# Optimization experiments

Hardware: AMD Instinct MI355X
Metric: run time of the kernel (lower is better)

The kernel has to match this reference:

```python
import jax, jax.numpy as jnp
import numpy as np

EMBED_DIM = 1024
NUM_HEADS = 16
HEAD_DIM = EMBED_DIM // NUM_HEADS


def setup_inputs() -> dict:
    key = jax.random.key(0)
    ks = jax.random.split(key, 9)
    B, S, E = 2, 2048, EMBED_DIM
    scale = 1.0 / np.sqrt(E)
    x = jax.random.normal(ks[0], (B, S, E), dtype=jnp.float32)
    Wq = jax.random.normal(ks[1], (E, E), dtype=jnp.float32) * scale
    bq = jax.random.normal(ks[2], (E,), dtype=jnp.float32) * 0.01
    Wk = jax.random.normal(ks[3], (E, E), dtype=jnp.float32) * scale
    bk = jax.random.normal(ks[4], (E,), dtype=jnp.float32) * 0.01
    Wv = jax.random.normal(ks[5], (E, E), dtype=jnp.float32) * scale
    bv = jax.random.normal(ks[6], (E,), dtype=jnp.float32) * 0.01
    Wo = jax.random.normal(ks[7], (E, E), dtype=jnp.float32) * scale
    bo = jax.random.normal(ks[8], (E,), dtype=jnp.float32) * 0.01
    return {"x": x, "Wq": Wq, "bq": bq, "Wk": Wk, "bk": bk,
            "Wv": Wv, "bv": bv, "Wo": Wo, "bo": bo}


def reference(x, Wq, bq, Wk, bk, Wv, bv, Wo, bo):
    B, S, E = x.shape
    H, D = NUM_HEADS, HEAD_DIM
    # projections (torch Linear: x @ W.T + b), reshape to (B, H, S, D)
    q = (x @ Wq.T + bq).reshape(B, S, H, D).transpose(0, 2, 1, 3)
    k = (x @ Wk.T + bk).reshape(B, S, H, D).transpose(0, 2, 1, 3)
    v = (x @ Wv.T + bv).reshape(B, S, H, D).transpose(0, 2, 1, 3)
    softmax_scale = 1.0 / np.sqrt(D)
    # (B, H, S, S) scores, causal mask, stable softmax
    scores = softmax_scale * jnp.einsum('bhsd,bhtd->bhst', q, k)
    causal = jnp.tril(jnp.ones((S, S), dtype=bool))  # True = keep
    scores = jnp.where(causal, scores, -jnp.inf)
    attn = jax.nn.softmax(scores, axis=-1)
    out = jnp.einsum('bhst,bhtd->bhsd', attn, v)  # (B, H, S, D)
    out = out.transpose(0, 2, 1, 3).reshape(B, S, E)
    return out @ Wo.T + bo
```

## Files before the change

### kernel.cpp

```cpp
#include <hip/hip_runtime.h>
#include <cstdint>
#include <cstddef>

#define SEQ   2048
#define BATCH 2
#define EMB   1024
#define NH    16
#define HD    64
#define MTOT  (BATCH * SEQ)
#define NX    (MTOT * EMB)
#define NW    (EMB * EMB)
#define QS    3072
#define SLOTF 8448
#define NSLOT 1152

typedef __bf16 bf16_t;
typedef __bf16 bf16x2 __attribute__((ext_vector_type(2)));
typedef __bf16 bf16x4 __attribute__((ext_vector_type(4)));
typedef __bf16 bf16x8 __attribute__((ext_vector_type(8)));
typedef float  f32x4  __attribute__((ext_vector_type(4)));
typedef float  f32x16 __attribute__((ext_vector_type(16)));

typedef __attribute__((address_space(1))) const void* as1cv;
typedef __attribute__((address_space(3))) void*       as3v;

__device__ __forceinline__ void async_cp16(const void* g, void* l) {
  __builtin_amdgcn_global_load_lds((as1cv)g, (as3v)l, 16, 0, 0);
}

__device__ __forceinline__ f32x16 mfma32(bf16x8 a, bf16x8 b, f32x16 c) {
  return __builtin_amdgcn_mfma_f32_32x32x16_bf16(a, b, c, 0, 0, 0);
}

__device__ __forceinline__ uint32_t pk2(float a, float b) {
  bf16x2 t; t[0] = (bf16_t)a; t[1] = (bf16_t)b;
  return __builtin_bit_cast(uint32_t, t);
}
__device__ __forceinline__ bf16x8 mk_frag(uint32_t x, uint32_t y,
                                          uint32_t z, uint32_t w) {
  uint4 u; u.x = x; u.y = y; u.z = z; u.w = w;
  return __builtin_bit_cast(bf16x8, u);
}

__device__ __forceinline__ void plane_swap(uint32_t& a, uint32_t& b) {
  asm("v_permlane32_swap_b32 %0, %1" : "+v"(a), "+v"(b));
}

__global__ __launch_bounds__(256) void cvt_all(
    const float* __restrict__ x,  const float* __restrict__ wq,
    const float* __restrict__ wk, const float* __restrict__ wv,
    const float* __restrict__ wo,
    bf16_t* __restrict__ xb,  bf16_t* __restrict__ wqb,
    bf16_t* __restrict__ wkb, bf16_t* __restrict__ wvb,
    bf16_t* __restrict__ wob) {
  long e = ((long)blockIdx.x * 256 + threadIdx.x) * 4;
  const float* s; bf16_t* d; long off;
  if (e < NX) { s = x; d = xb; off = e; }
  else {
    long e2 = e - NX;
    int w = (int)(e2 >> 20);
    off = e2 & (NW - 1);
    s = (w == 0) ? wq : (w == 1) ? wk : (w == 2) ? wv : wo;
    d = (w == 0) ? wqb : (w == 1) ? wkb : (w == 2) ? wvb : wob;
  }
  float4 v = *(const float4*)(s + off);
  bf16x4 o;
  o[0] = (bf16_t)v.x; o[1] = (bf16_t)v.y; o[2] = (bf16_t)v.z; o[3] = (bf16_t)v.w;
  *(bf16x4*)(d + off) = o;
}

__global__ __launch_bounds__(256) void vtrans(const bf16_t* __restrict__ QKV,
                                              bf16_t* __restrict__ VT) {
  const int hb = blockIdx.x;
  const int sb = blockIdx.y;
  const int h = hb & 15, b = hb >> 4;
  const int t = threadIdx.x;
  __shared__ __align__(16) bf16_t Ts[64 * 72];
  const bf16_t* Vp = QKV + ((size_t)(b * SEQ + sb * 64)) * QS + 2048 + h * HD;
  const int sr = t >> 4, d0 = (t & 15) * 4;
#pragma unroll
  for (int i = 0; i < 4; ++i) {
    bf16x4 v = *(const bf16x4*)(Vp + (size_t)(sr + 16 * i) * QS + d0);
    *(bf16x4*)&Ts[(sr + 16 * i) * 72 + d0] = v;
  }
  __syncthreads();
  const int d = t >> 2, tc = (t & 3) * 16;
  __align__(16) bf16_t out[16];
#pragma unroll
  for (int j = 0; j < 16; ++j) out[j] = Ts[(tc + j) * 72 + d];
  bf16_t* dst = VT + ((size_t)hb * HD + d) * SEQ + sb * 64 + tc;
  *(uint4*)(dst)     = *(uint4*)&out[0];
  *(uint4*)(dst + 8) = *(uint4*)&out[8];
}

template <typename OT, int BN, int CS>
__global__ __launch_bounds__(256) void gemm_f(
    const bf16_t* __restrict__ A, const bf16_t* __restrict__ Bw,
    const float* __restrict__ b0, const float* __restrict__ b1,
    const float* __restrict__ b2, OT* __restrict__ C) {
  constexpr int K = EMB, BK = 64;
  __shared__ __align__(16) bf16_t As[128 * BK];
  __shared__ __align__(16) bf16_t Bs[BN * BK];

  const int tid  = threadIdx.x;
  const int lane = tid & 63;
  const int wave = tid >> 6;
  const int l31  = lane & 31;
  const int hi   = lane >> 5;
  const int wm   = (wave >> 1) * 64;
  const int wn   = (wave & 1) * (BN / 2);
  const int m0   = blockIdx.y * 128;
  const int n0   = blockIdx.x * BN;

  const float* bias = (n0 < 1024) ? b0 : ((n0 < 2048) ? b1 : b2);

  const int row0 = tid >> 3, slot = tid & 7;
  const bf16_t* gA[4];
  const bf16_t* gB[BN / 32];
#pragma unroll
  for (int i = 0; i < 4; ++i)
    gA[i] = A + (size_t)(m0 + row0 + 32 * i) * K + (slot ^ (row0 & 7)) * 8;
#pragma unroll
  for (int i = 0; i < BN / 32; ++i)
    gB[i] = Bw + (size_t)(n0 + row0 + 32 * i) * K + (slot ^ (row0 & 7)) * 8;

  f32x16 acc[2][BN / 64] = {};
  const int sw = l31 & 7;

  for (int kk = 0; kk < K; kk += BK) {
#pragma unroll
    for (int i = 0; i < 4; ++i)
      async_cp16(gA[i] + kk, &As[(tid + 256 * i) * 8]);
#pragma unroll
    for (int i = 0; i < BN / 32; ++i)
      async_cp16(gB[i] + kk, &Bs[(tid + 256 * i) * 8]);
    __syncthreads();

#pragma unroll
    for (int ks = 0; ks < 4; ++ks) {
      const int js = ((ks * 2 + hi) ^ sw) * 8;
      bf16x8 af[2], bfr[BN / 64];
#pragma unroll
      for (int i = 0; i < 2; ++i)
        af[i] = *(const bf16x8*)&As[(wm + i * 32 + l31) * BK + js];
#pragma unroll
      for (int j = 0; j < BN / 64; ++j)
        bfr[j] = *(const bf16x8*)&Bs[(wn + j * 32 + l31) * BK + js];
#pragma unroll
      for (int i = 0; i < 2; ++i)
#pragma unroll
        for (int j = 0; j < BN / 64; ++j)
          acc[i][j] = mfma32(af[i], bfr[j], acc[i][j]);
    }
    __syncthreads();
  }

#pragma unroll
  for (int i = 0; i < 2; ++i)
#pragma unroll
    for (int j = 0; j < BN / 64; ++j) {
      const int col = n0 + wn + j * 32 + l31;
      const float bv = bias[col & 1023];
#pragma unroll
      for (int r = 0; r < 16; ++r) {
        const int row = m0 + wm + i * 32 + (r & 3) + 8 * (r >> 2) + 4 * hi;
        C[(size_t)row * CS + col] = (OT)(acc[i][j][r] + bv);
      }
    }
}

__global__ __launch_bounds__(256, 3) void attn128(
    const bf16_t* __restrict__ QKVg, const bf16_t* __restrict__ VTg,
    bf16_t* __restrict__ Og, float* __restrict__ Pb) {
  static const unsigned char St[40] = {
      3, 7, 7, 10, 11, 11, 11, 14, 14, 15, 15, 15, 15,
      6, 6, 9, 9, 10, 10, 12, 12, 13, 13, 13, 13, 14, 14,
      2, 5, 5, 8, 8, 8, 9, 12, 12,
      4, 4, 1, 0};
  static const unsigned char Ct[40] = {
      0, 0, 1, 0, 0, 1, 2, 0, 1, 0, 1, 2, 3,
      0, 1, 0, 1, 1, 2, 0, 1, 0, 1, 2, 3, 2, 3,
      0, 0, 1, 0, 1, 2, 2, 2, 3,
      0, 1, 0, 0};
  static const unsigned char cum[12] = {0, 2, 4, 6, 8, 11, 14, 17, 20, 24, 28, 32};

  const int hb  = blockIdx.x;
  const int y   = blockIdx.y;
  const int s   = St[y], c = Ct[y];
  const int nit = 2 * s + 2;
  const int nch = (s >> 2) + 1;
  const int bse = nit / nch;
  const int rem = nit - bse * nch;
  const int len = bse + (c < rem ? 1 : 0);
  const int it0 = c * bse + (c < rem ? c : rem);
  const int h = hb & 15, b = hb >> 4;
  const int tid = threadIdx.x;
  const int lane = tid & 63, wave = tid >> 6;
  const int l31 = lane & 31, hi = lane >> 5;

  __shared__ __align__(16) bf16_t Ks[2][64 * 72];
  __shared__ __align__(16) bf16_t VsT[2][64 * 72];
  __shared__ __align__(16) bf16_t Qs[128 * 64];

  const size_t base = ((size_t)b * SEQ) * QS + (size_t)h * HD;
  const bf16_t* Qb  = QKVg + base;
  const bf16_t* Kp  = QKVg + base + 1024;
  const bf16_t* VTp = VTg + (size_t)hb * HD * SEQ;

  const int kr0r = tid >> 3, kcol = (tid & 7) * 8;
  const int kr1r = kr0r + 32;
  const int lo0 = kr0r * 72 + kcol;
  const int lo1 = lo0 + 32 * 72;

  const int q0  = s * 128;
  const bf16_t* Qp = Qb + (size_t)q0 * QS;

  const bf16_t* Kn0 = Kp + (size_t)it0 * 64 * QS;
  const bf16_t* Vn0 = VTp + it0 * 64;
  uint4 kr0 = *(const uint4*)(Kn0 + (size_t)kr0r * QS + kcol);
  uint4 kr1 = *(const uint4*)(Kn0 + (size_t)kr1r * QS + kcol);
  uint4 vr0 = *(const uint4*)(Vn0 + (size_t)kr0r * SEQ + kcol);
  uint4 vr1 = *(const uint4*)(Vn0 + (size_t)kr1r * SEQ + kcol);

#pragma unroll
  for (int i = 0; i < 4; ++i) {
    const int cc = tid + 256 * i;
    *(uint4*)&Qs[(cc >> 3) * 64 + (cc & 7) * 8] =
        *(const uint4*)(Qp + (size_t)(cc >> 3) * QS + (cc & 7) * 8);
  }
  __syncthreads();

  bf16x8 qf[4];
#pragma unroll
  for (int kk = 0; kk < 4; ++kk)
    qf[kk] = *(const bf16x8*)&Qs[(32 * wave + l31) * 64 + kk * 16 + hi * 8];

  bf16x8 onef;
#pragma unroll
  for (int i = 0; i < 8; ++i) onef[i] = (bf16_t)1.0f;

  f32x16 acc_t0 = {}, acc_t1 = {};
  f32x16 acc_l  = {};

  for (int j = 0; j < len; ++j) {
    const int it = it0 + j;
    bf16_t* Kc = &Ks[j & 1][0];
    bf16_t* Vc = &VsT[j & 1][0];
    *(uint4*)&Kc[lo0] = kr0;
    *(uint4*)&Kc[lo1] = kr1;
    *(uint4*)&Vc[lo0] = vr0;
    *(uint4*)&Vc[lo1] = vr1;
    __syncthreads();

    if (j + 1 < len) {
      const bf16_t* Kn  = Kp + (size_t)(it + 1) * 64 * QS;
      const bf16_t* VTn = VTp + (it + 1) * 64;
      kr0 = *(const uint4*)(Kn + (size_t)kr0r * QS + kcol);
      kr1 = *(const uint4*)(Kn + (size_t)kr1r * QS + kcol);
      vr0 = *(const uint4*)(VTn + (size_t)kr0r * SEQ + kcol);
      vr1 = *(const uint4*)(VTn + (size_t)kr1r * SEQ + kcol);
    }

    const bool active = (64 * it <= q0 + 32 * wave + 31);
    if (active) {
      f32x16 s0 = {}, s1 = {};
      __builtin_amdgcn_s_setprio(1);
#pragma unroll
      for (int kk = 0; kk < 4; ++kk) {
        const bf16x8 kf0 = *(const bf16x8*)&Kc[l31 * 72 + kk * 16 + hi * 8];
        const bf16x8 kf1 =
            *(const bf16x8*)&Kc[(32 + l31) * 72 + kk * 16 + hi * 8];
        s0 = mfma32(kf0, qf[kk], s0);
        s1 = mfma32(kf1, qf[kk], s1);
      }
      __builtin_amdgcn_s_setprio(0);

      constexpr float SC2 = 0.18033688011112042f;
      if (it >= nit - 2) {
        const int qg = q0 + 32 * wave + l31;
        const int k0 = 64 * it + 4 * hi;
#pragma unroll
        for (int r = 0; r < 16; ++r) {
          const int key = k0 + (r & 3) + 8 * (r >> 2);
          float p0 = exp2f(__builtin_fmaf(s0[r], SC2, -8.f));
          float p1 = exp2f(__builtin_fmaf(s1[r], SC2, -8.f));
          if (key > qg) p0 = 0.f;
          if (key + 32 > qg) p1 = 0.f;
          s0[r] = p0; s1[r] = p1;
        }
      } else {
#pragma unroll
        for (int r = 0; r < 16; ++r) {
          s0[r] = exp2f(__builtin_fmaf(s0[r], SC2, -8.f));
          s1[r] = exp2f(__builtin_fmaf(s1[r], SC2, -8.f));
        }
      }

      bf16x8 pf[4];
#pragma unroll
      for (int kk = 0; kk < 4; ++kk) {
        const f32x16& g = (kk < 2) ? s0 : s1;
        const int bir = 8 * (kk & 1);
        uint32_t w0 = pk2(g[bir + 0], g[bir + 1]);
        uint32_t w1 = pk2(g[bir + 2], g[bir + 3]);
        uint32_t w2 = pk2(g[bir + 4], g[bir + 5]);
        uint32_t w3 = pk2(g[bir + 6], g[bir + 7]);
        plane_swap(w0, w2);
        plane_swap(w1, w3);
        pf[kk] = mk_frag(w0, w1, w2, w3);
      }

      __builtin_amdgcn_s_setprio(1);
#pragma unroll
      for (int kk = 0; kk < 4; ++kk) {
        const bf16x8 vf0 = *(const bf16x8*)&Vc[l31 * 72 + kk * 16 + hi * 8];
        const bf16x8 vf1 =
            *(const bf16x8*)&Vc[(32 + l31) * 72 + kk * 16 + hi * 8];
        acc_t0 = mfma32(vf0, pf[kk], acc_t0);
        acc_t1 = mfma32(vf1, pf[kk], acc_t1);
        acc_l  = mfma32(onef, pf[kk], acc_l);
      }
      __builtin_amdgcn_s_setprio(0);
    }
  }

  if (nch == 1) {
    const float inv = 1.f / acc_l[0];
    bf16_t* Ow = &Qs[(32 * wave) * 64];
#pragma unroll
    for (int aq = 0; aq < 4; ++aq)
#pragma unroll
      for (int cq = 0; cq < 4; cq += 2) {
        const int r = 4 * aq + cq;
        const int d = cq + 8 * aq + 4 * hi;
        *(uint32_t*)&Ow[l31 * 64 + d] =
            pk2(acc_t0[r] * inv, acc_t0[r + 1] * inv);
        *(uint32_t*)&Ow[l31 * 64 + d + 32] =
            pk2(acc_t1[r] * inv, acc_t1[r + 1] * inv);
      }
    bf16_t* Op = Og + ((size_t)b * SEQ + q0 + 32 * wave) * EMB + (size_t)h * HD;
#pragma unroll
    for (int i = 0; i < 4; ++i) {
      const int id = lane + 64 * i;
      const int row = id >> 3, col8 = (id & 7) * 8;
      *(uint4*)(Op + (size_t)row * EMB + col8) =
          *(const uint4*)&Ow[row * 64 + col8];
    }
  } else {
    float* P = Pb + (size_t)(hb * 36 + cum[s - 4] + c) * SLOTF;
#pragma unroll
    for (int i = 0; i < 4; ++i) {
      f32x4 v0, v1;
#pragma unroll
      for (int e = 0; e < 4; ++e) {
        v0[e] = acc_t0[4 * i + e];
        v1[e] = acc_t1[4 * i + e];
      }
      *(f32x4*)(P + (size_t)(i * 256 + tid) * 4)       = v0;
      *(f32x4*)(P + (size_t)((4 + i) * 256 + tid) * 4) = v1;
    }
    P[8192 + tid] = acc_l[0];
  }
}

__global__ __launch_bounds__(256) void attn_combine(
    const float* __restrict__ Pb, bf16_t* __restrict__ Og) {
  static const unsigned char cum[12] = {0, 2, 4, 6, 8, 11, 14, 17, 20, 24, 28, 32};
  const int hb = blockIdx.x, sp = blockIdx.y;
  const int s = sp + 4;
  const int h = hb & 15, b = hb >> 4;
  const int t = threadIdx.x;
  const int lane = t & 63, wave = t >> 6;
  const int l31 = lane & 31, hi = lane >> 5;
  const int nch = (s >> 2) + 1;
  const float* P0 = Pb + (size_t)(hb * 36 + cum[sp]) * SLOTF;

  f32x4 a[8] = {};
  float ls = 0.f;
  for (int c = 0; c < nch; ++c) {
    const float* P = P0 + (size_t)c * SLOTF;
#pragma unroll
    for (int i = 0; i < 8; ++i)
      a[i] += *(const f32x4*)(P + (size_t)(i * 256 + t) * 4);
    ls += P[8192 + t];
  }
  const float inv = 1.f / ls;

  __shared__ __align__(16) bf16_t Ow[128 * 64];
  bf16_t* Owp = &Ow[(32 * wave) * 64];
#pragma unroll
  for (int aq = 0; aq < 4; ++aq)
#pragma unroll
    for (int cq = 0; cq < 4; cq += 2) {
      const int d = cq + 8 * aq + 4 * hi;
      *(uint32_t*)&Owp[l31 * 64 + d] =
          pk2(a[aq][cq] * inv, a[aq][cq + 1] * inv);
      *(uint32_t*)&Owp[l31 * 64 + d + 32] =
          pk2(a[4 + aq][cq] * inv, a[4 + aq][cq + 1] * inv);
    }
  bf16_t* Op =
      Og + ((size_t)b * SEQ + 128 * s + 32 * wave) * EMB + (size_t)h * HD;
#pragma unroll
  for (int i = 0; i < 4; ++i) {
    const int id = lane + 64 * i;
    const int row = id >> 3, col8 = (id & 7) * 8;
    *(uint4*)(Op + (size_t)row * EMB + col8) =
        *(const uint4*)&Owp[row * 64 + col8];
  }
}

extern "C" void kernel_launch(void* const* d_in, const int* in_sizes, int n_in,
                              void* d_out, int out_size, void* d_ws,
                              size_t ws_size, hipStream_t stream) {
  const float* x  = (const float*)d_in[0];
  const float* Wq = (const float*)d_in[1];
  const float* bq = (const float*)d_in[2];
  const float* Wk = (const float*)d_in[3];
  const float* bk = (const float*)d_in[4];
  const float* Wv = (const float*)d_in[5];
  const float* bv = (const float*)d_in[6];
  const float* Wo = (const float*)d_in[7];
  const float* bo = (const float*)d_in[8];
  float* out = (float*)d_out;

  char* p = (char*)d_ws;
  bf16_t* xb   = (bf16_t*)p; p += (size_t)NX * 2;
  bf16_t* wqb  = (bf16_t*)p; p += (size_t)NW * 2;
  bf16_t* wkb  = (bf16_t*)p; p += (size_t)NW * 2;
  bf16_t* wvb  = (bf16_t*)p; p += (size_t)NW * 2;
  bf16_t* wob  = (bf16_t*)p; p += (size_t)NW * 2;
  bf16_t* qkvb = (bf16_t*)p; p += (size_t)NX * 3 * 2;
  bf16_t* ab   = (bf16_t*)p; p += (size_t)NX * 2;
  float*  pbuf = (float*)p;  p += (size_t)NSLOT * SLOTF * 4;
  bf16_t* vtb  = xb;

  const int ntot = NX + 4 * NW;
  cvt_all<<<dim3(ntot / 4 / 256), 256, 0, stream>>>(
      x, Wq, Wk, Wv, Wo, xb, wqb, wkb, wvb, wob);

  gemm_f<bf16_t, 128, QS><<<dim3(QS / 128, MTOT / 128), 256, 0, stream>>>(
      xb, wqb, bq, bk, bv, qkvb);

  vtrans<<<dim3(BATCH * NH, SEQ / 64), 256, 0, stream>>>(qkvb, vtb);

  attn128<<<dim3(BATCH * NH, 40), 256, 0, stream>>>(qkvb, vtb, ab, pbuf);

  attn_combine<<<dim3(BATCH * NH, 12), 256, 0, stream>>>(pbuf, ab);

  gemm_f<float, 64, EMB><<<dim3(EMB / 64, MTOT / 128), 256, 0, stream>>>(
      ab, wob, bo, bo, bo, out);
}
```

Before: 187.0 us.

## Replace QKV projection GEMM with 256x256-tile 8-wave pipelined kernel

Adds a new QKV projection GEMM that uses 256x256 output tiles, 512 threads (8 waves), and double-buffered LDS fed by async copies. Each K step is split into four phases that interleave prefetch of the next tile with MFMA work, using explicit barriers, vmcnt waits and s_setprio. The grid is also remapped so that blocks sharing data run close together. Larger tiles raise data reuse and the phased schedule is meant to hide global load latency, but the grid shrinks to 192 blocks and register and LDS pressure go up.

```diff
diff --git a/kernel.cpp b/kernel.cpp
--- a/kernel.cpp
+++ b/kernel.cpp
@@ -45,6 +45,9 @@
 __device__ __forceinline__ void plane_swap(uint32_t& a, uint32_t& b) {
   asm("v_permlane32_swap_b32 %0, %1" : "+v"(a), "+v"(b));
 }
+
+#define CFENCE asm volatile("" ::: "memory")
+#define BARRIER do { CFENCE; __builtin_amdgcn_s_barrier(); CFENCE; } while (0)
 
 __global__ __launch_bounds__(256) void cvt_all(
     const float* __restrict__ x,  const float* __restrict__ wq,
@@ -169,6 +172,120 @@
     }
 }
 
+__global__ __launch_bounds__(512, 2) void gemm8(
+    const bf16_t* __restrict__ A, const bf16_t* __restrict__ Bw,
+    const float* __restrict__ b0, const float* __restrict__ b1,
+    const float* __restrict__ b2, bf16_t* __restrict__ C) {
+  constexpr int K = EMB, BK = 64, NT = K / BK;
+  __shared__ __align__(16) bf16_t As[2][2][128 * BK];
+  __shared__ __align__(16) bf16_t Bs[2][2][128 * BK];
+
+  const int bid = blockIdx.y * 12 + blockIdx.x;
+  const int wg  = (bid & 7) * 24 + (bid >> 3);
+  const int bx  = wg >> 4, by = wg & 15;
+  const int n0  = bx * 256, m0 = by * 256;
+
+  const int tid  = threadIdx.x;
+  const int lane = tid & 63;
+  const int wave = tid >> 6;
+  const int l31  = lane & 31;
+  const int hi   = lane >> 5;
+  const int wm   = wave >> 2;
+  const int wn   = wave & 3;
+  const int sw   = l31 & 7;
+
+  const float* bias = (n0 < 1024) ? b0 : ((n0 < 2048) ? b1 : b2);
+
+  const int row = tid >> 3, slot = tid & 7;
+  const int scol = (slot ^ (row & 7)) * 8;
+  const bf16_t* gA[2][2];
+  const bf16_t* gB[2][2];
+#pragma unroll
+  for (int h = 0; h < 2; ++h)
+#pragma unroll
+    for (int i = 0; i < 2; ++i) {
+      gA[h][i] = A  + (size_t)(m0 + h * 128 + row + 64 * i) * K + scol;
+      gB[h][i] = Bw + (size_t)(n0 + h * 128 + row + 64 * i) * K + scol;
+    }
+
+#define STAGE_A8(par, h, kk) do {                                     \
+    async_cp16(gA[h][0] + (kk), &As[par][h][tid * 8]);                \
+    async_cp16(gA[h][1] + (kk), &As[par][h][(tid + 512) * 8]); } while (0)
+#define STAGE_B8(par, h, kk) do {                                     \
+    async_cp16(gB[h][0] + (kk), &Bs[par][h][tid * 8]);                \
+    async_cp16(gB[h][1] + (kk), &Bs[par][h][(tid + 512) * 8]); } while (0)
+
+  f32x16 acc[2][2][2] = {};
+
+#define PHASE8(qm, qn, STAGE_STMT, TAIL_STMT)                               \
+  do {                                                                      \
+    const bf16_t* Ab_ = &As[cur][wm][0];                                    \
+    const int bh_ = (wn * 64 + (qn) * 32) >> 7;                             \
+    const int br_ = ((wn * 64 + (qn) * 32) & 127) + l31;                    \
+    const bf16_t* Bb_ = &Bs[cur][bh_][0];                                   \
+    bf16x8 af0_[4], af1_[4], bf_[4];                                        \
+    _Pragma("unroll")                                                       \
+    for (int ks = 0; ks < 4; ++ks) {                                        \
+      const int js = ((ks * 2 + hi) ^ sw) * 8;                              \
+      af0_[ks] = *(const bf16x8*)&Ab_[((qm) * 64 + l31) * BK + js];         \
+      af1_[ks] = *(const bf16x8*)&Ab_[((qm) * 64 + 32 + l31) * BK + js];    \
+      bf_[ks]  = *(const bf16x8*)&Bb_[br_ * BK + js];                       \
+    }                                                                       \
+    STAGE_STMT;                                                             \
+    BARRIER;                                                                \
+    asm volatile("s_waitcnt lgkmcnt(0)" ::: "memory");                      \
+    __builtin_amdgcn_s_setprio(1);                                          \
+    _Pragma("unroll")                                                       \
+    for (int ks = 0; ks < 4; ++ks) {                                        \
+      acc[qm][0][qn] = mfma32(af0_[ks], bf_[ks], acc[qm][0][qn]);           \
+      acc[qm][1][qn] = mfma32(af1_[ks], bf_[ks], acc[qm][1][qn]);           \
+    }                                                                       \
+    __builtin_amdgcn_s_setprio(0);                                          \
+    TAIL_STMT;                                                              \
+    BARRIER;                                                                \
+  } while (0)
+
+  STAGE_B8(0, 0, 0);
+  STAGE_B8(0, 1, 0);
+  STAGE_A8(0, 0, 0);
+  STAGE_A8(0, 1, 0);
+  asm volatile("s_waitcnt vmcnt(2)" ::: "memory");
+  BARRIER;
+
+#pragma unroll 1
+  for (int t = 0; t < NT; ++t) {
+    const int cur = t & 1, nxt = cur ^ 1;
+    const int koff = (t + 1) * BK;
+    const bool pf = (t + 1 < NT);
+    PHASE8(0, 0, if (pf) STAGE_B8(nxt, 0, koff), );
+    PHASE8(0, 1, if (pf) STAGE_B8(nxt, 1, koff),
+           if (pf) { asm volatile("s_waitcnt vmcnt(4)" ::: "memory"); }
+           else    { asm volatile("s_waitcnt vmcnt(0)" ::: "memory"); });
+    PHASE8(1, 0, if (pf) STAGE_A8(nxt, 0, koff), );
+    PHASE8(1, 1, if (pf) STAGE_A8(nxt, 1, koff),
+           asm volatile("s_waitcnt vmcnt(2)" ::: "memory"));
+  }
+
+#pragma unroll
+  for (int qm = 0; qm < 2; ++qm)
+#pragma unroll
+    for (int f = 0; f < 2; ++f)
+#pragma unroll
+      for (int qn = 0; qn < 2; ++qn) {
+        const int col = n0 + wn * 64 + qn * 32 + l31;
+        const float bv = bias[col & 1023];
+#pragma unroll
+        for (int r = 0; r < 16; ++r) {
+          const int rw =
+              m0 + wm * 128 + qm * 64 + f * 32 + (r & 3) + 8 * (r >> 2) + 4 * hi;
+          C[(size_t)rw * QS + col] = (bf16_t)(acc[qm][f][qn][r] + bv);
+        }
+      }
+#undef PHASE8
+#undef STAGE_A8
+#undef STAGE_B8
+}
+
 __global__ __launch_bounds__(256, 3) void attn128(
     const bf16_t* __restrict__ QKVg, const bf16_t* __restrict__ VTg,
     bf16_t* __restrict__ Og, float* __restrict__ Pb) {
@@ -438,8 +555,7 @@
   cvt_all<<<dim3(ntot / 4 / 256), 256, 0, stream>>>(
       x, Wq, Wk, Wv, Wo, xb, wqb, wkb, wvb, wob);
 
-  gemm_f<bf16_t, 128, QS><<<dim3(QS / 128, MTOT / 128), 256, 0, stream>>>(
-      xb, wqb, bq, bk, bv, qkvb);
+  gemm8<<<dim3(12, 16), 512, 0, stream>>>(xb, wqb, bq, bk, bv, qkvb);
 
   vtrans<<<dim3(BATCH * NH, SEQ / 64), 256, 0, stream>>>(qkvb, vtb);
 
```

Result: slower. 199.4 us (+6.6%).

## Fuse split-K attention combine into last block and deepen K/V prefetch

Applied to the files above, without the earlier changes.

The attention main loop now keeps two register sets of K/V tiles, prefetching two iterations ahead. The next tile's LDS store is placed between the QK and PV phases, so each iteration needs one barrier instead of a store-then-sync pattern. The separate attn_combine kernel is removed: each split block writes its partials, bumps an atomic counter, and the last-arriving block sums the partials and writes the output. This saves a kernel launch and the re-read of its own partial, at the cost of extra registers, threadfence overhead and a counter reset in vtrans.

```diff
diff --git a/kernel.cpp b/kernel.cpp
--- a/kernel.cpp
+++ b/kernel.cpp
@@ -70,11 +70,16 @@
 }
 
 __global__ __launch_bounds__(256) void vtrans(const bf16_t* __restrict__ QKV,
-                                              bf16_t* __restrict__ VT) {
+                                              bf16_t* __restrict__ VT,
+                                              int* __restrict__ cnt) {
   const int hb = blockIdx.x;
   const int sb = blockIdx.y;
   const int h = hb & 15, b = hb >> 4;
   const int t = threadIdx.x;
+  if (hb == 0 && sb == 0) {
+    cnt[t] = 0;
+    if (t < 128) cnt[256 + t] = 0;
+  }
   __shared__ __align__(16) bf16_t Ts[64 * 72];
   const bf16_t* Vp = QKV + ((size_t)(b * SEQ + sb * 64)) * QS + 2048 + h * HD;
   const int sr = t >> 4, d0 = (t & 15) * 4;
@@ -171,7 +176,7 @@
 
 __global__ __launch_bounds__(256, 3) void attn128(
     const bf16_t* __restrict__ QKVg, const bf16_t* __restrict__ VTg,
-    bf16_t* __restrict__ Og, float* __restrict__ Pb) {
+    bf16_t* __restrict__ Og, float* __restrict__ Pb, int* __restrict__ cnt) {
   static const unsigned char St[40] = {
       3, 7, 7, 10, 11, 11, 11, 14, 14, 15, 15, 15, 15,
       6, 6, 9, 9, 10, 10, 12, 12, 13, 13, 13, 13, 14, 14,
@@ -201,6 +206,7 @@
   __shared__ __align__(16) bf16_t Ks[2][64 * 72];
   __shared__ __align__(16) bf16_t VsT[2][64 * 72];
   __shared__ __align__(16) bf16_t Qs[128 * 64];
+  __shared__ int oldS;
 
   const size_t base = ((size_t)b * SEQ) * QS + (size_t)h * HD;
   const bf16_t* Qb  = QKVg + base;
@@ -215,12 +221,18 @@
   const int q0  = s * 128;
   const bf16_t* Qp = Qb + (size_t)q0 * QS;
 
-  const bf16_t* Kn0 = Kp + (size_t)it0 * 64 * QS;
-  const bf16_t* Vn0 = VTp + it0 * 64;
-  uint4 kr0 = *(const uint4*)(Kn0 + (size_t)kr0r * QS + kcol);
-  uint4 kr1 = *(const uint4*)(Kn0 + (size_t)kr1r * QS + kcol);
-  uint4 vr0 = *(const uint4*)(Vn0 + (size_t)kr0r * SEQ + kcol);
-  uint4 vr1 = *(const uint4*)(Vn0 + (size_t)kr1r * SEQ + kcol);
+#define LOADT(itv, K0, K1, V0, V1) do {                                   \
+    const bf16_t* Kn_ = Kp + (size_t)(itv) * 64 * QS;                     \
+    const bf16_t* Vn_ = VTp + (size_t)(itv) * 64;                         \
+    K0 = *(const uint4*)(Kn_ + (size_t)kr0r * QS + kcol);                 \
+    K1 = *(const uint4*)(Kn_ + (size_t)kr1r * QS + kcol);                 \
+    V0 = *(const uint4*)(Vn_ + (size_t)kr0r * SEQ + kcol);                \
+    V1 = *(const uint4*)(Vn_ + (size_t)kr1r * SEQ + kcol);               \
+  } while (0)
+
+  uint4 kA0, kA1, vA0, vA1, kB0, kB1, vB0, vB1;
+  LOADT(it0, kA0, kA1, vA0, vA1);
+  LOADT(it0 + 1, kB0, kB1, vB0, vB1);
 
 #pragma unroll
   for (int i = 0; i < 4; ++i) {
@@ -228,6 +240,10 @@
     *(uint4*)&Qs[(cc >> 3) * 64 + (cc & 7) * 8] =
         *(const uint4*)(Qp + (size_t)(cc >> 3) * QS + (cc & 7) * 8);
   }
+  *(uint4*)&Ks[0][lo0] = kA0;
+  *(uint4*)&Ks[0][lo1] = kA1;
+  *(uint4*)&VsT[0][lo0] = vA0;
+  *(uint4*)&VsT[0][lo1] = vA1;
   __syncthreads();
 
   bf16x8 qf[4];
@@ -242,87 +258,88 @@
   f32x16 acc_t0 = {}, acc_t1 = {};
   f32x16 acc_l  = {};
 
-  for (int j = 0; j < len; ++j) {
-    const int it = it0 + j;
-    bf16_t* Kc = &Ks[j & 1][0];
-    bf16_t* Vc = &VsT[j & 1][0];
-    *(uint4*)&Kc[lo0] = kr0;
-    *(uint4*)&Kc[lo1] = kr1;
-    *(uint4*)&Vc[lo0] = vr0;
-    *(uint4*)&Vc[lo1] = vr1;
-    __syncthreads();
-
-    if (j + 1 < len) {
-      const bf16_t* Kn  = Kp + (size_t)(it + 1) * 64 * QS;
-      const bf16_t* VTn = VTp + (it + 1) * 64;
-      kr0 = *(const uint4*)(Kn + (size_t)kr0r * QS + kcol);
-      kr1 = *(const uint4*)(Kn + (size_t)kr1r * QS + kcol);
-      vr0 = *(const uint4*)(VTn + (size_t)kr0r * SEQ + kcol);
-      vr1 = *(const uint4*)(VTn + (size_t)kr1r * SEQ + kcol);
-    }
-
-    const bool active = (64 * it <= q0 + 32 * wave + 31);
-    if (active) {
-      f32x16 s0 = {}, s1 = {};
-      __builtin_amdgcn_s_setprio(1);
-#pragma unroll
-      for (int kk = 0; kk < 4; ++kk) {
-        const bf16x8 kf0 = *(const bf16x8*)&Kc[l31 * 72 + kk * 16 + hi * 8];
-        const bf16x8 kf1 =
-            *(const bf16x8*)&Kc[(32 + l31) * 72 + kk * 16 + hi * 8];
-        s0 = mfma32(kf0, qf[kk], s0);
-        s1 = mfma32(kf1, qf[kk], s1);
-      }
-      __builtin_amdgcn_s_setprio(0);
-
-      constexpr float SC2 = 0.18033688011112042f;
-      if (it >= nit - 2) {
-        const int qg = q0 + 32 * wave + l31;
-        const int k0 = 64 * it + 4 * hi;
-#pragma unroll
-        for (int r = 0; r < 16; ++r) {
-          const int key = k0 + (r & 3) + 8 * (r >> 2);
-          float p0 = exp2f(__builtin_fmaf(s0[r], SC2, -8.f));
-          float p1 = exp2f(__builtin_fmaf(s1[r], SC2, -8.f));
-          if (key > qg) p0 = 0.f;
-          if (key + 32 > qg) p1 = 0.f;
-          s0[r] = p0; s1[r] = p1;
-        }
-      } else {
-#pragma unroll
-        for (int r = 0; r < 16; ++r) {
-          s0[r] = exp2f(__builtin_fmaf(s0[r], SC2, -8.f));
-          s1[r] = exp2f(__builtin_fmaf(s1[r], SC2, -8.f));
-        }
-      }
-
-      bf16x8 pf[4];
-#pragma unroll
-      for (int kk = 0; kk < 4; ++kk) {
-        const f32x16& g = (kk < 2) ? s0 : s1;
-        const int bir = 8 * (kk & 1);
-        uint32_t w0 = pk2(g[bir + 0], g[bir + 1]);
-        uint32_t w1 = pk2(g[bir + 2], g[bir + 3]);
-        uint32_t w2 = pk2(g[bir + 4], g[bir + 5]);
-        uint32_t w3 = pk2(g[bir + 6], g[bir + 7]);
-        plane_swap(w0, w2);
-        plane_swap(w1, w3);
-        pf[kk] = mk_frag(w0, w1, w2, w3);
-      }
-
-      __builtin_amdgcn_s_setprio(1);
-#pragma unroll
-      for (int kk = 0; kk < 4; ++kk) {
-        const bf16x8 vf0 = *(const bf16x8*)&Vc[l31 * 72 + kk * 16 + hi * 8];
-        const bf16x8 vf1 =
-            *(const bf16x8*)&Vc[(32 + l31) * 72 + kk * 16 + hi * 8];
-        acc_t0 = mfma32(vf0, pf[kk], acc_t0);
-        acc_t1 = mfma32(vf1, pf[kk], acc_t1);
-        acc_l  = mfma32(onef, pf[kk], acc_l);
-      }
-      __builtin_amdgcn_s_setprio(0);
-    }
-  }
+#define ITER(jj, cb, CK0, CK1, CV0, CV1, NK0, NK1, NV0, NV1)              \
+  do {                                                                    \
+    const int it = it0 + (jj);                                            \
+    if ((jj) + 2 < len) LOADT(it + 2, CK0, CK1, CV0, CV1);                \
+    const bool active = (64 * it <= q0 + 32 * wave + 31);                 \
+    f32x16 s0 = {}, s1 = {};                                              \
+    bf16x8 pf[4];                                                         \
+    if (active) {                                                         \
+      __builtin_amdgcn_s_setprio(1);                                      \
+      _Pragma("unroll")                                                   \
+      for (int kk = 0; kk < 4; ++kk) {                                    \
+        const bf16x8 kf0 =                                                \
+            *(const bf16x8*)&Ks[cb][l31 * 72 + kk * 16 + hi * 8];         \
+        const bf16x8 kf1 =                                                \
+            *(const bf16x8*)&Ks[cb][(32 + l31) * 72 + kk * 16 + hi * 8];  \
+        s0 = mfma32(kf0, qf[kk], s0);                                     \
+        s1 = mfma32(kf1, qf[kk], s1);                                     \
+      }                                                                   \
+      __builtin_amdgcn_s_setprio(0);                                      \
+      constexpr float SC2 = 0.18033688011112042f;                         \
+      if (it >= nit - 2) {                                                \
+        const int qg = q0 + 32 * wave + l31;                              \
+        const int k0 = 64 * it + 4 * hi;                                  \
+        _Pragma("unroll")                                                 \
+        for (int r = 0; r < 16; ++r) {                                    \
+          const int key = k0 + (r & 3) + 8 * (r >> 2);                    \
+          float p0 = exp2f(__builtin_fmaf(s0[r], SC2, -8.f));             \
+          float p1 = exp2f(__builtin_fmaf(s1[r], SC2, -8.f));             \
+          if (key > qg) p0 = 0.f;                                         \
+          if (key + 32 > qg) p1 = 0.f;                                    \
+          s0[r] = p0; s1[r] = p1;                                         \
+        }                                                                 \
+      } else {                                                            \
+        _Pragma("unroll")                                                 \
+        for (int r = 0; r < 16; ++r) {                                    \
+          s0[r] = exp2f(__builtin_fmaf(s0[r], SC2, -8.f));                \
+          s1[r] = exp2f(__builtin_fmaf(s1[r], SC2, -8.f));                \
+        }                                                                 \
+      }                                                                   \
+      _Pragma("unroll")                                                   \
+      for (int kk = 0; kk < 4; ++kk) {                                    \
+        const f32x16& g = (kk < 2) ? s0 : s1;                             \
+        const int bir = 8 * (kk & 1);                                     \
+        uint32_t w0 = pk2(g[bir + 0], g[bir + 1]);                        \
+        uint32_t w1 = pk2(g[bir + 2], g[bir + 3]);                        \
+        uint32_t w2 = pk2(g[bir + 4], g[bir + 5]);                        \
+        uint32_t w3 = pk2(g[bir + 6], g[bir + 7]);                        \
+        plane_swap(w0, w2);                                               \
+        plane_swap(w1, w3);                                               \
+        pf[kk] = mk_frag(w0, w1, w2, w3);                                 \
+      }                                                                   \
+    }                                                                     \
+    if ((jj) + 1 < len) {         \
+      *(uint4*)&Ks[(cb) ^ 1][lo0] = NK0;                                  \
+      *(uint4*)&Ks[(cb) ^ 1][lo1] = NK1;                                  \
+      *(uint4*)&VsT[(cb) ^ 1][lo0] = NV0;                                 \
+      *(uint4*)&VsT[(cb) ^ 1][lo1] = NV1;                                 \
+    }                                                                     \
+    if (active) {                                                         \
+      __builtin_amdgcn_s_setprio(1);                                      \
+      _Pragma("unroll")                                                   \
+      for (int kk = 0; kk < 4; ++kk) {                                    \
+        const bf16x8 vf0 =                                                \
+            *(const bf16x8*)&VsT[cb][l31 * 72 + kk * 16 + hi * 8];        \
+        const bf16x8 vf1 =                                                \
+            *(const bf16x8*)&VsT[cb][(32 + l31) * 72 + kk * 16 + hi * 8]; \
+        acc_t0 = mfma32(vf0, pf[kk], acc_t0);                             \
+        acc_t1 = mfma32(vf1, pf[kk], acc_t1);                             \
+        acc_l  = mfma32(onef, pf[kk], acc_l);                             \
+      }                                                                   \
+      __builtin_amdgcn_s_setprio(0);                                      \
+    }                                                                     \
+    __syncthreads();                                                      \
+  } while (0)
+
+  for (int j = 0; j < len; j += 2) {
+    ITER(j, 0, kA0, kA1, vA0, vA1, kB0, kB1, vB0, vB1);
+    if (j + 1 < len)
+      ITER(j + 1, 1, kB0, kB1, vB0, vB1, kA0, kA1, vA0, vA1);
+  }
+#undef ITER
+#undef LOADT
 
   if (nch == 1) {
     const float inv = 1.f / acc_l[0];
@@ -346,60 +363,64 @@
       *(uint4*)(Op + (size_t)row * EMB + col8) =
           *(const uint4*)&Ow[row * 64 + col8];
     }
-  } else {
-    float* P = Pb + (size_t)(hb * 36 + cum[s - 4] + c) * SLOTF;
-#pragma unroll
-    for (int i = 0; i < 4; ++i) {
-      f32x4 v0, v1;
-#pragma unroll
-      for (int e = 0; e < 4; ++e) {
-        v0[e] = acc_t0[4 * i + e];
-        v1[e] = acc_t1[4 * i + e];
-      }
-      *(f32x4*)(P + (size_t)(i * 256 + tid) * 4)       = v0;
-      *(f32x4*)(P + (size_t)((4 + i) * 256 + tid) * 4) = v1;
-    }
-    P[8192 + tid] = acc_l[0];
-  }
-}
-
-__global__ __launch_bounds__(256) void attn_combine(
-    const float* __restrict__ Pb, bf16_t* __restrict__ Og) {
-  static const unsigned char cum[12] = {0, 2, 4, 6, 8, 11, 14, 17, 20, 24, 28, 32};
-  const int hb = blockIdx.x, sp = blockIdx.y;
-  const int s = sp + 4;
-  const int h = hb & 15, b = hb >> 4;
-  const int t = threadIdx.x;
-  const int lane = t & 63, wave = t >> 6;
-  const int l31 = lane & 31, hi = lane >> 5;
-  const int nch = (s >> 2) + 1;
+    return;
+  }
+
+  const int sp = s - 4;
+  float* P = Pb + (size_t)(hb * 36 + cum[sp] + c) * SLOTF;
+#pragma unroll
+  for (int i = 0; i < 4; ++i) {
+    f32x4 v0, v1;
+#pragma unroll
+    for (int e = 0; e < 4; ++e) {
+      v0[e] = acc_t0[4 * i + e];
+      v1[e] = acc_t1[4 * i + e];
+    }
+    *(f32x4*)(P + (size_t)(i * 256 + tid) * 4)       = v0;
+    *(f32x4*)(P + (size_t)((4 + i) * 256 + tid) * 4) = v1;
+  }
+  P[8192 + tid] = acc_l[0];
+
+  __threadfence();
+  __syncthreads();
+  if (tid == 0) oldS = atomicAdd(&cnt[hb * 12 + sp], 1);
+  __syncthreads();
+  if (oldS != nch - 1) return;
+  __threadfence();
+
+  float ls = acc_l[0];
+  f32x4 a2[8];
+#pragma unroll
+  for (int i = 0; i < 4; ++i) {
+#pragma unroll
+    for (int e = 0; e < 4; ++e) {
+      a2[i][e]     = acc_t0[4 * i + e];
+      a2[4 + i][e] = acc_t1[4 * i + e];
+    }
+  }
   const float* P0 = Pb + (size_t)(hb * 36 + cum[sp]) * SLOTF;
-
-  f32x4 a[8] = {};
-  float ls = 0.f;
-  for (int c = 0; c < nch; ++c) {
-    const float* P = P0 + (size_t)c * SLOTF;
+  for (int c2 = 0; c2 < nch; ++c2) {
+    if (c2 == c) continue;
+    const float* Pc = P0 + (size_t)c2 * SLOTF;
 #pragma unroll
     for (int i = 0; i < 8; ++i)
-      a[i] += *(const f32x4*)(P + (size_t)(i * 256 + t) * 4);
-    ls += P[8192 + t];
+      a2[i] += *(const f32x4*)(Pc + (size_t)(i * 256 + tid) * 4);
+    ls += Pc[8192 + tid];
   }
   const float inv = 1.f / ls;
 
-  __shared__ __align__(16) bf16_t Ow[128 * 64];
-  bf16_t* Owp = &Ow[(32 * wave) * 64];
+  bf16_t* Owp = &Qs[(32 * wave) * 64];
 #pragma unroll
   for (int aq = 0; aq < 4; ++aq)
 #pragma unroll
     for (int cq = 0; cq < 4; cq += 2) {
       const int d = cq + 8 * aq + 4 * hi;
       *(uint32_t*)&Owp[l31 * 64 + d] =
-          pk2(a[aq][cq] * inv, a[aq][cq + 1] * inv);
+          pk2(a2[aq][cq] * inv, a2[aq][cq + 1] * inv);
       *(uint32_t*)&Owp[l31 * 64 + d + 32] =
-          pk2(a[4 + aq][cq] * inv, a[4 + aq][cq + 1] * inv);
-    }
-  bf16_t* Op =
-      Og + ((size_t)b * SEQ + 128 * s + 32 * wave) * EMB + (size_t)h * HD;
+          pk2(a2[4 + aq][cq] * inv, a2[4 + aq][cq + 1] * inv);
+    }
+  bf16_t* Op = Og + ((size_t)b * SEQ + q0 + 32 * wave) * EMB + (size_t)h * HD;
 #pragma unroll
   for (int i = 0; i < 4; ++i) {
     const int id = lane + 64 * i;
@@ -432,6 +453,7 @@
   bf16_t* qkvb = (bf16_t*)p; p += (size_t)NX * 3 * 2;
   bf16_t* ab   = (bf16_t*)p; p += (size_t)NX * 2;
   float*  pbuf = (float*)p;  p += (size_t)NSLOT * SLOTF * 4;
+  int*    cnt  = (int*)p;    p += 384 * 4;
   bf16_t* vtb  = xb;
 
   const int ntot = NX + 4 * NW;
@@ -441,11 +463,9 @@
   gemm_f<bf16_t, 128, QS><<<dim3(QS / 128, MTOT / 128), 256, 0, stream>>>(
       xb, wqb, bq, bk, bv, qkvb);
 
-  vtrans<<<dim3(BATCH * NH, SEQ / 64), 256, 0, stream>>>(qkvb, vtb);
-
-  attn128<<<dim3(BATCH * NH, 40), 256, 0, stream>>>(qkvb, vtb, ab, pbuf);
-
-  attn_combine<<<dim3(BATCH * NH, 12), 256, 0, stream>>>(pbuf, ab);
+  vtrans<<<dim3(BATCH * NH, SEQ / 64), 256, 0, stream>>>(qkvb, vtb, cnt);
+
+  attn128<<<dim3(BATCH * NH, 40), 256, 0, stream>>>(qkvb, vtb, ab, pbuf, cnt);
 
   gemm_f<float, 64, EMB><<<dim3(EMB / 64, MTOT / 128), 256, 0, stream>>>(
       ab, wob, bo, bo, bo, out);
```

After: 406.9 us. 118% more time.

## Fuse V transpose into QKV GEMM epilogue and widen output GEMM tile

Applied to the files above, without the earlier changes.

Adds a dedicated QKV GEMM whose epilogue, for V column blocks, stages the biased tile through shared memory and writes V already transposed into a separate buffer. This removes the separate vtrans kernel launch and its extra global read/write of V. The V transpose buffer now gets its own workspace region instead of aliasing xb. The output projection GEMM also switches from BN=64 to BN=128, which halves its grid and may lower occupancy.

```diff
diff --git a/kernel.cpp b/kernel.cpp
--- a/kernel.cpp
+++ b/kernel.cpp
@@ -69,28 +69,113 @@
   *(bf16x4*)(d + off) = o;
 }
 
-__global__ __launch_bounds__(256) void vtrans(const bf16_t* __restrict__ QKV,
-                                              bf16_t* __restrict__ VT) {
-  const int hb = blockIdx.x;
-  const int sb = blockIdx.y;
-  const int h = hb & 15, b = hb >> 4;
-  const int t = threadIdx.x;
-  __shared__ __align__(16) bf16_t Ts[64 * 72];
-  const bf16_t* Vp = QKV + ((size_t)(b * SEQ + sb * 64)) * QS + 2048 + h * HD;
-  const int sr = t >> 4, d0 = (t & 15) * 4;
-#pragma unroll
-  for (int i = 0; i < 4; ++i) {
-    bf16x4 v = *(const bf16x4*)(Vp + (size_t)(sr + 16 * i) * QS + d0);
-    *(bf16x4*)&Ts[(sr + 16 * i) * 72 + d0] = v;
-  }
-  __syncthreads();
-  const int d = t >> 2, tc = (t & 3) * 16;
-  __align__(16) bf16_t out[16];
-#pragma unroll
-  for (int j = 0; j < 16; ++j) out[j] = Ts[(tc + j) * 72 + d];
-  bf16_t* dst = VT + ((size_t)hb * HD + d) * SEQ + sb * 64 + tc;
-  *(uint4*)(dst)     = *(uint4*)&out[0];
-  *(uint4*)(dst + 8) = *(uint4*)&out[8];
+__global__ __launch_bounds__(256) void gemm_qkv(
+    const bf16_t* __restrict__ A, const bf16_t* __restrict__ Bw,
+    const float* __restrict__ b0, const float* __restrict__ b1,
+    const float* __restrict__ b2, bf16_t* __restrict__ C,
+    bf16_t* __restrict__ VT) {
+  constexpr int K = EMB, BK = 64, BN = 128;
+  __shared__ __align__(16) char smem[32768];
+  bf16_t* As = (bf16_t*)smem;
+  bf16_t* Bs = (bf16_t*)(smem + 16384);
+
+  const int tid  = threadIdx.x;
+  const int lane = tid & 63;
+  const int wave = tid >> 6;
+  const int l31  = lane & 31;
+  const int hi   = lane >> 5;
+  const int wm   = (wave >> 1) * 64;
+  const int wn   = (wave & 1) * (BN / 2);
+  const int m0   = blockIdx.y * 128;
+  const int n0   = blockIdx.x * BN;
+
+  const float* bias = (n0 < 1024) ? b0 : ((n0 < 2048) ? b1 : b2);
+
+  const int row0 = tid >> 3, slot = tid & 7;
+  const bf16_t* gA[4];
+  const bf16_t* gB[4];
+#pragma unroll
+  for (int i = 0; i < 4; ++i)
+    gA[i] = A + (size_t)(m0 + row0 + 32 * i) * K + (slot ^ (row0 & 7)) * 8;
+#pragma unroll
+  for (int i = 0; i < 4; ++i)
+    gB[i] = Bw + (size_t)(n0 + row0 + 32 * i) * K + (slot ^ (row0 & 7)) * 8;
+
+  f32x16 acc[2][2] = {};
+  const int sw = l31 & 7;
+
+  for (int kk = 0; kk < K; kk += BK) {
+#pragma unroll
+    for (int i = 0; i < 4; ++i)
+      async_cp16(gA[i] + kk, &As[(tid + 256 * i) * 8]);
+#pragma unroll
+    for (int i = 0; i < 4; ++i)
+      async_cp16(gB[i] + kk, &Bs[(tid + 256 * i) * 8]);
+    __syncthreads();
+
+#pragma unroll
+    for (int ks = 0; ks < 4; ++ks) {
+      const int js = ((ks * 2 + hi) ^ sw) * 8;
+      bf16x8 af[2], bfr[2];
+#pragma unroll
+      for (int i = 0; i < 2; ++i)
+        af[i] = *(const bf16x8*)&As[(wm + i * 32 + l31) * BK + js];
+#pragma unroll
+      for (int j = 0; j < 2; ++j)
+        bfr[j] = *(const bf16x8*)&Bs[(wn + j * 32 + l31) * BK + js];
+#pragma unroll
+      for (int i = 0; i < 2; ++i)
+#pragma unroll
+        for (int j = 0; j < 2; ++j)
+          acc[i][j] = mfma32(af[i], bfr[j], acc[i][j]);
+    }
+    __syncthreads();
+  }
+
+  if (n0 < 2048) {
+#pragma unroll
+    for (int i = 0; i < 2; ++i)
+#pragma unroll
+      for (int j = 0; j < 2; ++j) {
+        const int col = n0 + wn + j * 32 + l31;
+        const float bv = bias[col & 1023];
+#pragma unroll
+        for (int r = 0; r < 16; ++r) {
+          const int row = m0 + wm + i * 32 + (r & 3) + 8 * (r >> 2) + 4 * hi;
+          C[(size_t)row * QS + col] = (bf16_t)(acc[i][j][r] + bv);
+        }
+      }
+  } else {
+    const int h0 = (n0 - 2048) >> 6;
+    const int bb = m0 >> 11;
+    const int srow0 = m0 & 2047;
+    bf16_t* Ts = (bf16_t*)smem;
+    for (int hh = 0; hh < 2; ++hh) {
+      if ((wave & 1) == hh) {
+#pragma unroll
+        for (int i = 0; i < 2; ++i)
+#pragma unroll
+          for (int j = 0; j < 2; ++j) {
+            const int d = j * 32 + l31;
+            const float bv = bias[(n0 + wn + j * 32 + l31) & 1023];
+#pragma unroll
+            for (int r = 0; r < 16; ++r) {
+              const int row = wm + i * 32 + (r & 3) + 8 * (r >> 2) + 4 * hi;
+              Ts[d * 136 + row] = (bf16_t)(acc[i][j][r] + bv);
+            }
+          }
+      }
+      __syncthreads();
+      const int d = tid >> 2, ch = (tid & 3) * 32;
+      bf16_t* dst =
+          VT + ((size_t)((bb * 16 + h0 + hh) * 64 + d)) * SEQ + srow0 + ch;
+      const bf16_t* src = &Ts[d * 136 + ch];
+#pragma unroll
+      for (int q = 0; q < 4; ++q)
+        *(uint4*)(dst + q * 8) = *(const uint4*)(src + q * 8);
+      __syncthreads();
+    }
+  }
 }
 
 template <typename OT, int BN, int CS>
@@ -216,7 +301,7 @@
   const bf16_t* Qp = Qb + (size_t)q0 * QS;
 
   const bf16_t* Kn0 = Kp + (size_t)it0 * 64 * QS;
-  const bf16_t* Vn0 = VTp + it0 * 64;
+  const bf16_t* Vn0 = VTp + (size_t)it0 * 64;
   uint4 kr0 = *(const uint4*)(Kn0 + (size_t)kr0r * QS + kcol);
   uint4 kr1 = *(const uint4*)(Kn0 + (size_t)kr1r * QS + kcol);
   uint4 vr0 = *(const uint4*)(Vn0 + (size_t)kr0r * SEQ + kcol);
@@ -431,22 +516,20 @@
   bf16_t* wob  = (bf16_t*)p; p += (size_t)NW * 2;
   bf16_t* qkvb = (bf16_t*)p; p += (size_t)NX * 3 * 2;
   bf16_t* ab   = (bf16_t*)p; p += (size_t)NX * 2;
+  bf16_t* vtb  = (bf16_t*)p; p += (size_t)NX * 2;
   float*  pbuf = (float*)p;  p += (size_t)NSLOT * SLOTF * 4;
-  bf16_t* vtb  = xb;
 
   const int ntot = NX + 4 * NW;
   cvt_all<<<dim3(ntot / 4 / 256), 256, 0, stream>>>(
       x, Wq, Wk, Wv, Wo, xb, wqb, wkb, wvb, wob);
 
-  gemm_f<bf16_t, 128, QS><<<dim3(QS / 128, MTOT / 128), 256, 0, stream>>>(
-      xb, wqb, bq, bk, bv, qkvb);
-
-  vtrans<<<dim3(BATCH * NH, SEQ / 64), 256, 0, stream>>>(qkvb, vtb);
+  gemm_qkv<<<dim3(QS / 128, MTOT / 128), 256, 0, stream>>>(
+      xb, wqb, bq, bk, bv, qkvb, vtb);
 
   attn128<<<dim3(BATCH * NH, 40), 256, 0, stream>>>(qkvb, vtb, ab, pbuf);
 
   attn_combine<<<dim3(BATCH * NH, 12), 256, 0, stream>>>(pbuf, ab);
 
-  gemm_f<float, 64, EMB><<<dim3(EMB / 64, MTOT / 128), 256, 0, stream>>>(
+  gemm_f<float, 128, EMB><<<dim3(EMB / 128, MTOT / 128), 256, 0, stream>>>(
       ab, wob, bo, bo, bo, out);
 }
```

Result: slower. 210.4 us (+12.5%).
